# Optimization experiments

Hardware: AMD Instinct MI355X
Metric: run time of the kernel (lower is better)

Reference implementation:

```python
import jax, jax.numpy as jnp
import numpy as np

N_NODES = 100000
N_EDGES = 1600000
IN_DIM, HID_DIM, OUT_DIM = 128, 64, 64


def setup_inputs() -> dict:
    key = jax.random.key(0)
    ks = jax.random.split(key, 7)
    x = jax.random.normal(ks[0], (N_NODES, IN_DIM), dtype=jnp.float32)
    edge_index = jax.random.randint(ks[1], (2, N_EDGES), 0, N_NODES, dtype=jnp.int64)
    user_idx = jax.random.randint(ks[2], (N_NODES,), 0, N_NODES, dtype=jnp.int64)
    W1 = jax.random.normal(ks[3], (IN_DIM, HID_DIM), dtype=jnp.float32) * (1.0 / np.sqrt(IN_DIM))
    b1 = jax.random.normal(ks[4], (HID_DIM,), dtype=jnp.float32) * 0.02
    W2 = jax.random.normal(ks[5], (HID_DIM, OUT_DIM), dtype=jnp.float32) * (1.0 / np.sqrt(HID_DIM))
    b2 = jax.random.normal(ks[6], (OUT_DIM,), dtype=jnp.float32) * 0.02
    return {"x": x, "edge_index": edge_index, "user_idx": user_idx,
            "W1": W1, "b1": b1, "W2": W2, "b2": b2}


def _gcn_conv(x, edge_index, W, b):
    # PyG GCNConv: linear transform, add self-loops, sym-normalized aggregation.
    N = x.shape[0]
    h = x @ W  # [N, F_out]
    loop = jnp.arange(N, dtype=edge_index.dtype)
    src = jnp.concatenate([edge_index[0], loop])  # [E+N]
    dst = jnp.concatenate([edge_index[1], loop])
    deg = jax.ops.segment_sum(jnp.ones(src.shape[0], dtype=h.dtype), dst, num_segments=N)
    dis = jnp.where(deg > 0, jax.lax.rsqrt(jnp.maximum(deg, 1.0)), 0.0)  # deg^{-1/2}
    norm = dis[src] * dis[dst]  # [E+N]
    msg = h[src] * norm[:, None]  # gather + scale
    out = jax.ops.segment_sum(msg, dst, num_segments=N)  # scatter-add at targets
    return out + b


def _scatter_mean(x, idx, dim_size):
    s = jax.ops.segment_sum(x, idx, num_segments=dim_size)
    cnt = jax.ops.segment_sum(jnp.ones(x.shape[0], dtype=x.dtype), idx, num_segments=dim_size)
    return jnp.where(cnt[:, None] > 0, s / jnp.maximum(cnt[:, None], 1.0), 0.0)


def reference(x, edge_index, user_idx, W1, b1, W2, b2):
    h = _gcn_conv(x, edge_index, W1, b1)
    h = jax.nn.relu(h)
    # dropout is identity in eval mode
    h = _gcn_conv(h, edge_index, W2, b2)
    return _scatter_mean(h, user_idx, h.shape[0])
```

## Files before the change

### kernel.cpp

```cpp
#include <hip/hip_runtime.h>
#include <hip/hip_bf16.h>


#define FEAT 64
#define INDIM 128

#define SCAN_BS 256
#define SCAN_ELEMS 8
#define SCAN_CHUNK (SCAN_BS * SCAN_ELEMS)

#define BIN_SHIFT 9
#define BIN_R 512
#define BIN_TILE 2048
#define BH_TILE 2048

typedef __attribute__((ext_vector_type(8))) short short8;
typedef __attribute__((ext_vector_type(4))) float f32x4;

__device__ __forceinline__ unsigned short f2bf(float f) {
    unsigned u = __float_as_uint(f);
    unsigned r = u + 0x7FFFu + ((u >> 16) & 1u);
    return (unsigned short)(r >> 16);
}
__device__ __forceinline__ float bf2f(unsigned short v) {
    return __uint_as_float(((unsigned)v) << 16);
}


__global__ __launch_bounds__(256) void k_bhist(const int* __restrict__ dst,
                                               int* __restrict__ gbc,
                                               const int* __restrict__ uidx,
                                               float* __restrict__ cntf,
                                               int E, int N, int KB) {
    __shared__ int h[256];
    const int tid = threadIdx.x;
    h[tid] = 0;
    __syncthreads();
    const int base = blockIdx.x * BH_TILE;
    #pragma unroll
    for (int t = 0; t < BH_TILE / 256; ++t) {
        int e = base + t * 256 + tid;
        if (e < E) {
            int d = dst[e];
            if ((unsigned)d < (unsigned)N) atomicAdd(&h[d >> BIN_SHIFT], 1);
        }
    }
    int i = blockIdx.x * 256 + tid;
    if (i < N) {
        int u = uidx[i];
        if ((unsigned)u < (unsigned)N) atomicAdd(&cntf[u], 1.0f);
    }
    __syncthreads();
    if (tid < KB && h[tid]) atomicAdd(&gbc[tid], h[tid]);
}

__global__ __launch_bounds__(256) void k_bscan(const int* __restrict__ gbc,
                                               int* __restrict__ bb,
                                               int* __restrict__ bcur,
                                               int* __restrict__ rpN, int KB) {
    __shared__ int lds[256];
    const int tid = threadIdx.x;
    int v = (tid < KB) ? gbc[tid] : 0;
    lds[tid] = v;
    __syncthreads();
    for (int d = 1; d < 256; d <<= 1) {
        int t = (tid >= d) ? lds[tid - d] : 0;
        __syncthreads();
        lds[tid] += t;
        __syncthreads();
    }
    int excl = lds[tid] - v;
    if (tid < KB) { bb[tid] = excl; bcur[tid] = excl; }
    if (tid == 255) { bb[KB] = lds[255]; *rpN = lds[255]; }
}

__global__ __launch_bounds__(256) void k_binA(const int* __restrict__ src,
                                              const int* __restrict__ dst,
                                              int* __restrict__ bcur,
                                              unsigned* __restrict__ pairs,
                                              int E, int N, int KB) {
    __shared__ unsigned lbuf[BIN_TILE];
    __shared__ unsigned short bkt[BIN_TILE];
    __shared__ int lcnt[256];
    __shared__ int loff[256];
    __shared__ int lbase[256];
    __shared__ int tot;
    const int tid = threadIdx.x;
    const int base = blockIdx.x * BIN_TILE;

    lcnt[tid] = 0;
    __syncthreads();

    int mys[BIN_TILE / 256], myd[BIN_TILE / 256], myb[BIN_TILE / 256];
    #pragma unroll
    for (int t = 0; t < BIN_TILE / 256; ++t) {
        int e = base + t * 256 + tid;
        int s = 0, d = -1;
        if (e < E) { s = src[e]; d = dst[e]; }
        if ((unsigned)d >= (unsigned)N) d = -1;
        if ((unsigned)s >= (unsigned)N) s = 0;
        mys[t] = s; myd[t] = d;
        myb[t] = (d >= 0) ? (d >> BIN_SHIFT) : -1;
        if (myb[t] >= 0) atomicAdd(&lcnt[myb[t]], 1);
    }
    __syncthreads();

    int v = lcnt[tid];
    loff[tid] = v;
    __syncthreads();
    for (int d = 1; d < 256; d <<= 1) {
        int t2 = (tid >= d) ? loff[tid - d] : 0;
        __syncthreads();
        loff[tid] += t2;
        __syncthreads();
    }
    if (tid == 255) tot = loff[255];
    int excl = loff[tid] - v;
    __syncthreads();
    loff[tid] = excl;
    lcnt[tid] = excl;
    if (tid < KB && v > 0) lbase[tid] = atomicAdd(&bcur[tid], v);
    __syncthreads();

    #pragma unroll
    for (int t = 0; t < BIN_TILE / 256; ++t) {
        if (myb[t] >= 0) {
            int pos = atomicAdd(&lcnt[myb[t]], 1);
            lbuf[pos] = ((unsigned)mys[t] << BIN_SHIFT) | (unsigned)(myd[t] & (BIN_R - 1));
            bkt[pos] = (unsigned short)myb[t];
        }
    }
    __syncthreads();

    const int T = tot;
    for (int i = tid; i < T; i += 256) {
        int b = bkt[i];
        pairs[lbase[b] + (i - loff[b])] = lbuf[i];
    }
}

__global__ __launch_bounds__(1024) void k_binB2(const unsigned* __restrict__ pairs,
                                                const int* __restrict__ bb,
                                                int* __restrict__ rp,
                                                int* __restrict__ col,
                                                float* __restrict__ dis, int N) {
    __shared__ int cnt[BIN_R];
    __shared__ int cur[BIN_R];
    __shared__ int ssum[256];
    const int tid = threadIdx.x;
    const int b = blockIdx.x;
    const int n0 = b << BIN_SHIFT;
    const int n1 = min(n0 + BIN_R, N);
    const int nn = n1 - n0;
    const int e0 = bb[b];
    const int e1 = bb[b + 1];

    for (int i = tid; i < nn; i += 1024) cnt[i] = 0;
    __syncthreads();
    for (int i = e0 + tid; i < e1; i += 1024) {
        atomicAdd(&cnt[pairs[i] & (BIN_R - 1)], 1);
    }
    __syncthreads();

    const int i0 = 2 * tid;
    int c0 = 0, c1 = 0;
    if (tid < 256) {
        c0 = (i0     < nn) ? cnt[i0]     : 0;
        c1 = (i0 + 1 < nn) ? cnt[i0 + 1] : 0;
        ssum[tid] = c0 + c1;
    }
    __syncthreads();
    for (int d = 1; d < 256; d <<= 1) {
        int t = 0;
        if (tid < 256 && tid >= d) t = ssum[tid - d];
        __syncthreads();
        if (tid < 256) ssum[tid] += t;
        __syncthreads();
    }
    if (tid < 256) {
        int excl = ssum[tid] - (c0 + c1);
        if (i0 < nn) {
            cur[i0] = e0 + excl;
            rp[n0 + i0] = e0 + excl;
            dis[n0 + i0] = rsqrtf((float)c0 + 1.0f);
        }
        if (i0 + 1 < nn) {
            cur[i0 + 1] = e0 + excl + c0;
            rp[n0 + i0 + 1] = e0 + excl + c0;
            dis[n0 + i0 + 1] = rsqrtf((float)c1 + 1.0f);
        }
    }
    __syncthreads();

    for (int i = e0 + tid; i < e1; i += 1024) {
        unsigned p = pairs[i];
        int pos = atomicAdd(&cur[p & (BIN_R - 1)], 1);
        col[pos] = (int)(p >> BIN_SHIFT);
    }
}


__global__ __launch_bounds__(256) void k_hist(const int* __restrict__ dst,
                                              int* __restrict__ cntE, int E, int N) {
    int e = blockIdx.x * 256 + threadIdx.x;
    if (e < E) {
        int d = dst[e];
        if ((unsigned)d < (unsigned)N) atomicAdd(&cntE[d], 1);
    }
}
__global__ __launch_bounds__(256) void k_dis(const int* __restrict__ cntE,
                                             float* __restrict__ dis, int N) {
    int i = blockIdx.x * 256 + threadIdx.x;
    if (i < N) dis[i] = rsqrtf((float)cntE[i] + 1.0f);
}
__global__ __launch_bounds__(SCAN_BS) void k_scan1(const int* __restrict__ c,
                                                   int* __restrict__ rp,
                                                   int* __restrict__ ptot, int N) {
    __shared__ int lds[SCAN_BS];
    const int base = blockIdx.x * SCAN_CHUNK;
    const int tb = base + threadIdx.x * SCAN_ELEMS;
    int vals[SCAN_ELEMS];
    int s = 0;
    #pragma unroll
    for (int k = 0; k < SCAN_ELEMS; ++k) {
        int idx = tb + k;
        int v = (idx < N) ? c[idx] : 0;
        vals[k] = s;
        s += v;
    }
    lds[threadIdx.x] = s;
    __syncthreads();
    for (int d = 1; d < SCAN_BS; d <<= 1) {
        int v = (threadIdx.x >= d) ? lds[threadIdx.x - d] : 0;
        __syncthreads();
        lds[threadIdx.x] += v;
        __syncthreads();
    }
    int toff = (threadIdx.x == 0) ? 0 : lds[threadIdx.x - 1];
    #pragma unroll
    for (int k = 0; k < SCAN_ELEMS; ++k) {
        int idx = tb + k;
        if (idx < N) rp[idx] = toff + vals[k];
    }
    if (threadIdx.x == SCAN_BS - 1) ptot[blockIdx.x] = lds[SCAN_BS - 1];
}
__global__ __launch_bounds__(1024) void k_scan2(int* __restrict__ ptot,
                                                int* __restrict__ poff,
                                                int* __restrict__ rpN, int nb) {
    __shared__ int lds[1024];
    int tid = threadIdx.x;
    lds[tid] = (tid < nb) ? ptot[tid] : 0;
    __syncthreads();
    for (int d = 1; d < 1024; d <<= 1) {
        int v = (tid >= d) ? lds[tid - d] : 0;
        __syncthreads();
        lds[tid] += v;
        __syncthreads();
    }
    if (tid < nb) poff[tid] = (tid == 0) ? 0 : lds[tid - 1];
    if (tid == nb - 1) *rpN = lds[tid];
}
__global__ __launch_bounds__(SCAN_BS) void k_scan3(int* __restrict__ rp,
                                                   const int* __restrict__ poff, int N) {
    int off = poff[blockIdx.x];
    const int tb = blockIdx.x * SCAN_CHUNK + threadIdx.x * SCAN_ELEMS;
    #pragma unroll
    for (int k = 0; k < SCAN_ELEMS; ++k) {
        int idx = tb + k;
        if (idx < N) rp[idx] += off;
    }
}
__global__ __launch_bounds__(256) void k_fill(const int* __restrict__ src,
                                              const int* __restrict__ dst,
                                              const int* __restrict__ rp,
                                              int* __restrict__ tmp,
                                              int* __restrict__ col, int E, int N) {
    int e = blockIdx.x * 256 + threadIdx.x;
    if (e >= E) return;
    int s = src[e], d = dst[e];
    if ((unsigned)s >= (unsigned)N) s = 0;
    if ((unsigned)d >= (unsigned)N) return;
    int r = atomicAdd(&tmp[d], 1);
    col[rp[d] + r] = s;
}

__global__ __launch_bounds__(256) void k_ucnt(const int* __restrict__ uidx,
                                              float* __restrict__ cntf, int N) {
    int i = blockIdx.x * 256 + threadIdx.x;
    if (i < N) {
        int u = uidx[i];
        if ((unsigned)u < (unsigned)N) atomicAdd(&cntf[u], 1.0f);
    }
}


__global__ __launch_bounds__(256) void k_gemm1(const float* __restrict__ x,
                                               const float* __restrict__ W,
                                               const float* __restrict__ scale,
                                               unsigned short* __restrict__ out, int N) {
    __shared__ short wf[4 * 4 * 64 * 8];
    const int tid = threadIdx.x;
    if (blockIdx.x == 0 && tid < 8) {
        uint4 z; z.x = 0; z.y = 0; z.z = 0; z.w = 0;
        *reinterpret_cast<uint4*>(out + (long)N * FEAT + tid * 8) = z;
    }
    for (int i = tid; i < INDIM * FEAT; i += 256) {
        int k = i >> 6, n = i & 63;
        int ct = n >> 4, kc = k >> 5, r = k & 31;
        int owner = ((r >> 3) << 4) | (n & 15);
        wf[(((ct << 2) | kc) * 64 + owner) * 8 + (r & 7)] = (short)f2bf(W[i]);
    }
    __syncthreads();

    const int lane = tid & 63;
    const int m = lane & 15, q = lane >> 4;
    const int row0 = blockIdx.x * 64 + (tid >> 6) * 16;

    short8 bfr[4][4];
    #pragma unroll
    for (int ct = 0; ct < 4; ++ct)
        #pragma unroll
        for (int kc = 0; kc < 4; ++kc)
            bfr[ct][kc] = *reinterpret_cast<const short8*>(&wf[(((ct << 2) | kc) * 64 + lane) * 8]);

    int gr = row0 + m;
    int rl = gr < N ? gr : (N - 1);
    const float* xp = x + (long)rl * INDIM + q * 8;

    f32x4 acc[4] = {{0,0,0,0},{0,0,0,0},{0,0,0,0},{0,0,0,0}};
    #pragma unroll
    for (int kc = 0; kc < 4; ++kc) {
        float4 v0 = *reinterpret_cast<const float4*>(xp + kc * 32);
        float4 v1 = *reinterpret_cast<const float4*>(xp + kc * 32 + 4);
        short8 a;
        a[0]=(short)f2bf(v0.x); a[1]=(short)f2bf(v0.y); a[2]=(short)f2bf(v0.z); a[3]=(short)f2bf(v0.w);
        a[4]=(short)f2bf(v1.x); a[5]=(short)f2bf(v1.y); a[6]=(short)f2bf(v1.z); a[7]=(short)f2bf(v1.w);
        #pragma unroll
        for (int ct = 0; ct < 4; ++ct)
            acc[ct] = __builtin_amdgcn_mfma_f32_16x16x32_bf16(a, bfr[ct][kc], acc[ct], 0, 0, 0);
    }

    #pragma unroll
    for (int reg = 0; reg < 4; ++reg) {
        int row = row0 + q * 4 + reg;
        if (row < N) {
            float sc = scale[row];
            #pragma unroll
            for (int ct = 0; ct < 4; ++ct)
                out[(long)row * FEAT + ct * 16 + m] = f2bf(acc[ct][reg] * sc);
        }
    }
}

__global__ __launch_bounds__(256) void k_gemm2(const unsigned short* __restrict__ h,
                                               const float* __restrict__ W,
                                               const float* __restrict__ scale,
                                               unsigned short* __restrict__ out, int N) {
    __shared__ short wf[4 * 2 * 64 * 8];
    const int tid = threadIdx.x;
    if (blockIdx.x == 0 && tid < 8) {
        uint4 z; z.x = 0; z.y = 0; z.z = 0; z.w = 0;
        *reinterpret_cast<uint4*>(out + (long)N * FEAT + tid * 8) = z;
    }
    for (int i = tid; i < FEAT * FEAT; i += 256) {
        int k = i >> 6, n = i & 63;
        int ct = n >> 4, kc = k >> 5, r = k & 31;
        int owner = ((r >> 3) << 4) | (n & 15);
        wf[(((ct << 1) | kc) * 64 + owner) * 8 + (r & 7)] = (short)f2bf(W[i]);
    }
    __syncthreads();

    const int lane = tid & 63;
    const int m = lane & 15, q = lane >> 4;
    const int row0 = blockIdx.x * 64 + (tid >> 6) * 16;

    short8 bfr[4][2];
    #pragma unroll
    for (int ct = 0; ct < 4; ++ct)
        #pragma unroll
        for (int kc = 0; kc < 2; ++kc)
            bfr[ct][kc] = *reinterpret_cast<const short8*>(&wf[(((ct << 1) | kc) * 64 + lane) * 8]);

    int gr = row0 + m;
    int rl = gr < N ? gr : (N - 1);
    const unsigned short* hp = h + (long)rl * FEAT + q * 8;

    f32x4 acc[4] = {{0,0,0,0},{0,0,0,0},{0,0,0,0},{0,0,0,0}};
    #pragma unroll
    for (int kc = 0; kc < 2; ++kc) {
        short8 a = *reinterpret_cast<const short8*>(hp + kc * 32);
        #pragma unroll
        for (int ct = 0; ct < 4; ++ct)
            acc[ct] = __builtin_amdgcn_mfma_f32_16x16x32_bf16(a, bfr[ct][kc], acc[ct], 0, 0, 0);
    }

    #pragma unroll
    for (int reg = 0; reg < 4; ++reg) {
        int row = row0 + q * 4 + reg;
        if (row < N) {
            float sc = scale[row];
            #pragma unroll
            for (int ct = 0; ct < 4; ++ct)
                out[(long)row * FEAT + ct * 16 + m] = f2bf(acc[ct][reg] * sc);
        }
    }
}


#define ACC8(r)                                                                  \
    a0 += bf2f((unsigned short)(r).x);                                           \
    a1 += bf2f((unsigned short)((r).x >> 16));                                   \
    a2 += bf2f((unsigned short)(r).y);                                           \
    a3 += bf2f((unsigned short)((r).y >> 16));                                   \
    a4 += bf2f((unsigned short)(r).z);                                           \
    a5 += bf2f((unsigned short)((r).z >> 16));                                   \
    a6 += bf2f((unsigned short)(r).w);                                           \
    a7 += bf2f((unsigned short)((r).w >> 16));

#define AGG_BODY(SELF_INIT)                                                      \
    const int lane = threadIdx.x & 63;                                           \
    const int wv = threadIdx.x >> 6;                                             \
    const int p  = lane >> 4;                                                    \
    const int s  = (lane >> 3) & 1;                                              \
    const int ol = lane & 7;                                                     \
    const int i  = blockIdx.x * 16 + wv * 4 + p;                                 \
    const bool valid = (i < N);                                                  \
    const int jb = valid ? rp[i] : 0;                                            \
    const int je = valid ? rp[i + 1] : 0;                                        \
    float a0=0.f,a1=0.f,a2=0.f,a3=0.f,a4=0.f,a5=0.f,a6=0.f,a7=0.f;               \
    if (valid && s == 0) { SELF_INIT }                                           \
    for (int j0 = jb; j0 < je; j0 += 16) {                                       \
        int j1 = j0 + s;                                                         \
        int c1 = (j1      < je) ? col[j1]      : N;                              \
        int c2 = (j1 + 2  < je) ? col[j1 + 2]  : N;                              \
        int c3 = (j1 + 4  < je) ? col[j1 + 4]  : N;                              \
        int c4 = (j1 + 6  < je) ? col[j1 + 6]  : N;                              \
        int c5 = (j1 + 8  < je) ? col[j1 + 8]  : N;                              \
        int c6 = (j1 + 10 < je) ? col[j1 + 10] : N;                              \
        int c7 = (j1 + 12 < je) ? col[j1 + 12] : N;                              \
        int c8 = (j1 + 14 < je) ? col[j1 + 14] : N;                              \
        uint4 r1 = *reinterpret_cast<const uint4*>(A + (long)c1 * FEAT + 8 * ol);\
        uint4 r2 = *reinterpret_cast<const uint4*>(A + (long)c2 * FEAT + 8 * ol);\
        uint4 r3 = *reinterpret_cast<const uint4*>(A + (long)c3 * FEAT + 8 * ol);\
        uint4 r4 = *reinterpret_cast<const uint4*>(A + (long)c4 * FEAT + 8 * ol);\
        uint4 r5 = *reinterpret_cast<const uint4*>(A + (long)c5 * FEAT + 8 * ol);\
        uint4 r6 = *reinterpret_cast<const uint4*>(A + (long)c6 * FEAT + 8 * ol);\
        uint4 r7 = *reinterpret_cast<const uint4*>(A + (long)c7 * FEAT + 8 * ol);\
        uint4 r8 = *reinterpret_cast<const uint4*>(A + (long)c8 * FEAT + 8 * ol);\
        ACC8(r1)                                                                 \
        ACC8(r2)                                                                 \
        ACC8(r3)                                                                 \
        ACC8(r4)                                                                 \
        ACC8(r5)                                                                 \
        ACC8(r6)                                                                 \
        ACC8(r7)                                                                 \
        ACC8(r8)                                                                 \
    }                                                                            \
    a0 += __shfl_xor(a0, 8);  a1 += __shfl_xor(a1, 8);                           \
    a2 += __shfl_xor(a2, 8);  a3 += __shfl_xor(a3, 8);                           \
    a4 += __shfl_xor(a4, 8);  a5 += __shfl_xor(a5, 8);                           \
    a6 += __shfl_xor(a6, 8);  a7 += __shfl_xor(a7, 8);

__global__ __launch_bounds__(256) void k_agg1(const unsigned short* __restrict__ A,
                                              const int* __restrict__ rp,
                                              const int* __restrict__ col,
                                              const float* __restrict__ dis,
                                              const float* __restrict__ bias,
                                              unsigned short* __restrict__ H, int N) {
    AGG_BODY(
        uint4 rv = *reinterpret_cast<const uint4*>(A + (long)i * FEAT + 8 * ol);
        a0 = bf2f((unsigned short)rv.x); a1 = bf2f((unsigned short)(rv.x >> 16));
        a2 = bf2f((unsigned short)rv.y); a3 = bf2f((unsigned short)(rv.y >> 16));
        a4 = bf2f((unsigned short)rv.z); a5 = bf2f((unsigned short)(rv.z >> 16));
        a6 = bf2f((unsigned short)rv.w); a7 = bf2f((unsigned short)(rv.w >> 16));
    )
    if (s == 0 && valid) {
        float di = dis[i];
        float4 b4a = *reinterpret_cast<const float4*>(bias + 8 * ol);
        float4 b4b = *reinterpret_cast<const float4*>(bias + 8 * ol + 4);
        uint4 o;
        o.x = (unsigned)f2bf(fmaxf(fmaf(di, a0, b4a.x), 0.f))
            | ((unsigned)f2bf(fmaxf(fmaf(di, a1, b4a.y), 0.f)) << 16);
        o.y = (unsigned)f2bf(fmaxf(fmaf(di, a2, b4a.z), 0.f))
            | ((unsigned)f2bf(fmaxf(fmaf(di, a3, b4a.w), 0.f)) << 16);
        o.z = (unsigned)f2bf(fmaxf(fmaf(di, a4, b4b.x), 0.f))
            | ((unsigned)f2bf(fmaxf(fmaf(di, a5, b4b.y), 0.f)) << 16);
        o.w = (unsigned)f2bf(fmaxf(fmaf(di, a6, b4b.z), 0.f))
            | ((unsigned)f2bf(fmaxf(fmaf(di, a7, b4b.w), 0.f)) << 16);
        *reinterpret_cast<uint4*>(H + (long)i * FEAT + 8 * ol) = o;
    }
}

__global__ __launch_bounds__(256) void k_agg2s(const unsigned short* __restrict__ A,
                                               const int* __restrict__ rp,
                                               const int* __restrict__ col,
                                               const float* __restrict__ dis,
                                               const float* __restrict__ bias,
                                               const int* __restrict__ uidx,
                                               const float* __restrict__ cntf,
                                               float* __restrict__ S, int N) {
    __shared__ float sbuf[4][4][65];
    AGG_BODY(
        uint4 rv = *reinterpret_cast<const uint4*>(A + (long)i * FEAT + 8 * ol);
        a0 = bf2f((unsigned short)rv.x); a1 = bf2f((unsigned short)(rv.x >> 16));
        a2 = bf2f((unsigned short)rv.y); a3 = bf2f((unsigned short)(rv.y >> 16));
        a4 = bf2f((unsigned short)rv.z); a5 = bf2f((unsigned short)(rv.z >> 16));
        a6 = bf2f((unsigned short)rv.w); a7 = bf2f((unsigned short)(rv.w >> 16));
    )
    if (s == 0) {
        float* dl = &sbuf[wv][p][8 * ol];
        dl[0] = a0; dl[1] = a1; dl[2] = a2; dl[3] = a3;
        dl[4] = a4; dl[5] = a5; dl[6] = a6; dl[7] = a7;
    }
    __syncthreads();
    const int base4 = blockIdx.x * 16 + wv * 4;
    const float bl = bias[lane];
    #pragma unroll
    for (int pp = 0; pp < 4; ++pp) {
        int node = base4 + pp;
        if (node < N) {
            int u = uidx[node];
            if ((unsigned)u < (unsigned)N) {
                float c = cntf[u];
                float wgt = (c > 0.f) ? (1.0f / c) : 0.f;
                float di = dis[node];
                float v = sbuf[wv][pp][lane];
                atomicAdd(&S[(long)u * FEAT + lane], wgt * fmaf(di, v, bl));
            }
        }
    }
}

extern "C" void kernel_launch(void* const* d_in, const int* in_sizes, int n_in,
                              void* d_out, int out_size, void* d_ws, size_t ws_size,
                              hipStream_t stream) {
    const float* x   = (const float*)d_in[0];
    const int* edge  = (const int*)d_in[1];
    const int* uidx  = (const int*)d_in[2];
    const float* W1  = (const float*)d_in[3];
    const float* b1  = (const float*)d_in[4];
    const float* W2  = (const float*)d_in[5];
    const float* b2  = (const float*)d_in[6];
    float* out       = (float*)d_out;

    const int N = in_sizes[2];
    const int E = in_sizes[1] / 2;
    const int* src = edge;
    const int* dst = edge + E;

    const size_t fbuf = (size_t)N * FEAT * sizeof(float);
    const size_t abuf = (size_t)(N + 1) * FEAT * sizeof(unsigned short);
    const int gE   = (E + 255) / 256;
    const int gN   = (N + 255) / 256;
    const int gN16 = (N + 15) / 16;
    const int gG   = (N + 63) / 64;
    const int nbScan = (N + SCAN_CHUNK - 1) / SCAN_CHUNK;
    const int KB = (N + BIN_R - 1) >> BIN_SHIFT;

    auto align256 = [](size_t v) { return (v + 255) & ~(size_t)255; };

    char* w = (char*)d_ws;
    size_t o = 0;
    float* dis  = (float*)(w + o); o = align256(o + (size_t)N * 4);
    float* cntf = (float*)(w + o); o = align256(o + (size_t)N * 4);
    int*   rp   = (int*)  (w + o); o = align256(o + (size_t)(N + 1) * 4);
    int*   cntE = (int*)  (w + o); o = align256(o + (size_t)N * 4);
    int*   ptot = (int*)  (w + o); o = align256(o + (size_t)1024 * 4);
    int*   poff = (int*)  (w + o); o = align256(o + (size_t)1024 * 4);
    int*   col  = (int*)  (w + o); o = align256(o + (size_t)E * 4);
    size_t apsz = (size_t)E * 4 > abuf ? (size_t)E * 4 : abuf;
    char*  Ap   = w + o;           o = align256(o + apsz);
    const size_t need = o;
    int* gbc  = cntE;
    int* bb   = ptot;
    int* bcur = poff;
    unsigned* pairs = (unsigned*)Ap;
    unsigned short* A = (unsigned short*)Ap;
    unsigned short* Hb = (unsigned short*)out;

    if (ws_size >= need && KB <= 256 && N <= (1 << (32 - BIN_SHIFT - 1))) {
        hipMemsetAsync(gbc, 0, (size_t)KB * 4, stream);
        hipMemsetAsync(cntf, 0, (size_t)N * 4, stream);
        k_bhist<<<(E + BH_TILE - 1) / BH_TILE, 256, 0, stream>>>(dst, gbc, uidx, cntf, E, N, KB);
        k_bscan<<<1, 256, 0, stream>>>(gbc, bb, bcur, rp + N, KB);
        k_binA <<<(E + BIN_TILE - 1) / BIN_TILE, 256, 0, stream>>>(src, dst, bcur, pairs, E, N, KB);
        k_binB2<<<KB, 1024, 0, stream>>>(pairs, bb, rp, col, dis, N);

        k_gemm1<<<gG, 256, 0, stream>>>(x, W1, dis, A, N);
        k_agg1 <<<gN16, 256, 0, stream>>>(A, rp, col, dis, b1, Hb, N);

        k_gemm2<<<gG, 256, 0, stream>>>(Hb, W2, dis, A, N);
        hipMemsetAsync(out, 0, fbuf, stream);
        k_agg2s<<<gN16, 256, 0, stream>>>(A, rp, col, dis, b2, uidx, cntf, out, N);
    } else {
        hipMemsetAsync(cntE, 0, (size_t)N * 4, stream);
        k_hist <<<gE, 256, 0, stream>>>(dst, cntE, E, N);
        k_dis  <<<gN, 256, 0, stream>>>(cntE, dis, N);
        k_scan1<<<nbScan, SCAN_BS, 0, stream>>>(cntE, rp, ptot, N);
        k_scan2<<<1, 1024, 0, stream>>>(ptot, poff, rp + N, nbScan);
        k_scan3<<<nbScan, SCAN_BS, 0, stream>>>(rp, poff, N);
        hipMemsetAsync(cntE, 0, (size_t)N * 4, stream);
        k_fill <<<gE, 256, 0, stream>>>(src, dst, rp, cntE, col, E, N);
        hipMemsetAsync(cntf, 0, (size_t)N * 4, stream);
        k_ucnt <<<gN, 256, 0, stream>>>(uidx, cntf, N);
        k_gemm1<<<gG, 256, 0, stream>>>(x, W1, dis, A, N);
        k_agg1 <<<gN16, 256, 0, stream>>>(A, rp, col, dis, b1, Hb, N);
        k_gemm2<<<gG, 256, 0, stream>>>(Hb, W2, dis, A, N);
        hipMemsetAsync(out, 0, fbuf, stream);
        k_agg2s<<<gN16, 256, 0, stream>>>(A, rp, col, dis, b2, uidx, cntf, out, N);
    }
}
```

Measured before the change: 276.1 us.

## Fuse layer-2 GEMM into layer-1 aggregation and fold output zeroing into histogram

Adds k_agg1f, which aggregates layer 1, applies bias and ReLU into shared memory, then multiplies by W2 with MFMA bf16 instructions and writes the scaled layer-2 input into a new workspace buffer. This removes the separate k_gemm2 launch and the global round trip of the hidden activations. The output zeroing memset moves into the k_bhist grid-stride loop, and the two small memsets become one contiguous memset after the workspace is reordered. It needs an extra workspace buffer and keeps the old path as a fallback when the workspace is too small. Each agg block now reloads and repacks all of W2 into shared memory.

```diff
diff --git a/kernel.cpp b/kernel.cpp
--- a/kernel.cpp
+++ b/kernel.cpp
@@ -31,6 +31,7 @@
                                                int* __restrict__ gbc,
                                                const int* __restrict__ uidx,
                                                float* __restrict__ cntf,
+                                               uint4* __restrict__ outz, long nz4,
                                                int E, int N, int KB) {
     __shared__ int h[256];
     const int tid = threadIdx.x;
@@ -49,6 +50,12 @@
     if (i < N) {
         int u = uidx[i];
         if ((unsigned)u < (unsigned)N) atomicAdd(&cntf[u], 1.0f);
+    }
+    if (outz) {
+        uint4 z; z.x = 0; z.y = 0; z.z = 0; z.w = 0;
+        const long stride = (long)gridDim.x * 256;
+        for (long idx = (long)blockIdx.x * 256 + tid; idx < nz4; idx += stride)
+            outz[idx] = z;
     }
     __syncthreads();
     if (tid < KB && h[tid]) atomicAdd(&gbc[tid], h[tid]);
@@ -491,6 +498,74 @@
     }
 }
 
+__global__ __launch_bounds__(256) void k_agg1f(const unsigned short* __restrict__ A,
+                                               const int* __restrict__ rp,
+                                               const int* __restrict__ col,
+                                               const float* __restrict__ dis,
+                                               const float* __restrict__ bias,
+                                               const float* __restrict__ W2,
+                                               unsigned short* __restrict__ A2, int N) {
+    __shared__ short wf[4 * 2 * 64 * 8];
+    __shared__ unsigned short hh[16][72];
+    __shared__ float dl[16];
+    const int tid = threadIdx.x;
+    for (int ii = tid; ii < FEAT * FEAT; ii += 256) {
+        int k = ii >> 6, n = ii & 63;
+        int ct = n >> 4, kc = k >> 5, r = k & 31;
+        int owner = ((r >> 3) << 4) | (n & 15);
+        wf[(((ct << 1) | kc) * 64 + owner) * 8 + (r & 7)] = (short)f2bf(W2[ii]);
+    }
+    const int base16 = blockIdx.x * 16;
+    if (tid < 16) {
+        int node = base16 + tid;
+        dl[tid] = (node < N) ? dis[node] : 0.f;
+    }
+    if (blockIdx.x == 0 && tid >= 32 && tid < 40) {
+        uint4 z; z.x = 0; z.y = 0; z.z = 0; z.w = 0;
+        *reinterpret_cast<uint4*>(A2 + (long)N * FEAT + (tid - 32) * 8) = z;
+    }
+
+    AGG_BODY(
+        uint4 rv = *reinterpret_cast<const uint4*>(A + (long)i * FEAT + 8 * ol);
+        a0 = bf2f((unsigned short)rv.x); a1 = bf2f((unsigned short)(rv.x >> 16));
+        a2 = bf2f((unsigned short)rv.y); a3 = bf2f((unsigned short)(rv.y >> 16));
+        a4 = bf2f((unsigned short)rv.z); a5 = bf2f((unsigned short)(rv.z >> 16));
+        a6 = bf2f((unsigned short)rv.w); a7 = bf2f((unsigned short)(rv.w >> 16));
+    )
+    if (s == 0 && valid) {
+        float di = dis[i];
+        float4 b4a = *reinterpret_cast<const float4*>(bias + 8 * ol);
+        float4 b4b = *reinterpret_cast<const float4*>(bias + 8 * ol + 4);
+        uint4 o;
+        o.x = (unsigned)f2bf(fmaxf(fmaf(di, a0, b4a.x), 0.f))
+            | ((unsigned)f2bf(fmaxf(fmaf(di, a1, b4a.y), 0.f)) << 16);
+        o.y = (unsigned)f2bf(fmaxf(fmaf(di, a2, b4a.z), 0.f))
+            | ((unsigned)f2bf(fmaxf(fmaf(di, a3, b4a.w), 0.f)) << 16);
+        o.z = (unsigned)f2bf(fmaxf(fmaf(di, a4, b4b.x), 0.f))
+            | ((unsigned)f2bf(fmaxf(fmaf(di, a5, b4b.y), 0.f)) << 16);
+        o.w = (unsigned)f2bf(fmaxf(fmaf(di, a6, b4b.z), 0.f))
+            | ((unsigned)f2bf(fmaxf(fmaf(di, a7, b4b.w), 0.f)) << 16);
+        *reinterpret_cast<uint4*>(&hh[wv * 4 + p][8 * ol]) = o;
+    }
+    __syncthreads();
+
+    const int m = lane & 15, q = lane >> 4;
+    short8 af0 = *reinterpret_cast<const short8*>(&hh[m][q * 8]);
+    short8 af1 = *reinterpret_cast<const short8*>(&hh[m][32 + q * 8]);
+    short8 bf0 = *reinterpret_cast<const short8*>(&wf[(((wv << 1) | 0) * 64 + lane) * 8]);
+    short8 bf1 = *reinterpret_cast<const short8*>(&wf[(((wv << 1) | 1) * 64 + lane) * 8]);
+    f32x4 acc = {0, 0, 0, 0};
+    acc = __builtin_amdgcn_mfma_f32_16x16x32_bf16(af0, bf0, acc, 0, 0, 0);
+    acc = __builtin_amdgcn_mfma_f32_16x16x32_bf16(af1, bf1, acc, 0, 0, 0);
+    #pragma unroll
+    for (int reg = 0; reg < 4; ++reg) {
+        int node = q * 4 + reg;
+        int row = base16 + node;
+        if (row < N)
+            A2[(long)row * FEAT + wv * 16 + m] = f2bf(acc[reg] * dl[node]);
+    }
+}
+
 __global__ __launch_bounds__(256) void k_agg2s(const unsigned short* __restrict__ A,
                                                const int* __restrict__ rp,
                                                const int* __restrict__ col,
@@ -508,9 +583,9 @@
         a6 = bf2f((unsigned short)rv.w); a7 = bf2f((unsigned short)(rv.w >> 16));
     )
     if (s == 0) {
-        float* dl = &sbuf[wv][p][8 * ol];
-        dl[0] = a0; dl[1] = a1; dl[2] = a2; dl[3] = a3;
-        dl[4] = a4; dl[5] = a5; dl[6] = a6; dl[7] = a7;
+        float* dst = &sbuf[wv][p][8 * ol];
+        dst[0] = a0; dst[1] = a1; dst[2] = a2; dst[3] = a3;
+        dst[4] = a4; dst[5] = a5; dst[6] = a6; dst[7] = a7;
     }
     __syncthreads();
     const int base4 = blockIdx.x * 16 + wv * 4;
@@ -554,6 +629,7 @@
     const int gN   = (N + 255) / 256;
     const int gN16 = (N + 15) / 16;
     const int gG   = (N + 63) / 64;
+    const int gBH  = (E + BH_TILE - 1) / BH_TILE;
     const int nbScan = (N + SCAN_CHUNK - 1) / SCAN_CHUNK;
     const int KB = (N + BIN_R - 1) >> BIN_SHIFT;
 
@@ -563,14 +639,17 @@
     size_t o = 0;
     float* dis  = (float*)(w + o); o = align256(o + (size_t)N * 4);
     float* cntf = (float*)(w + o); o = align256(o + (size_t)N * 4);
+    int*   cntE = (int*)  (w + o); o = align256(o + (size_t)N * 4);
     int*   rp   = (int*)  (w + o); o = align256(o + (size_t)(N + 1) * 4);
-    int*   cntE = (int*)  (w + o); o = align256(o + (size_t)N * 4);
     int*   ptot = (int*)  (w + o); o = align256(o + (size_t)1024 * 4);
     int*   poff = (int*)  (w + o); o = align256(o + (size_t)1024 * 4);
     int*   col  = (int*)  (w + o); o = align256(o + (size_t)E * 4);
     size_t apsz = (size_t)E * 4 > abuf ? (size_t)E * 4 : abuf;
     char*  Ap   = w + o;           o = align256(o + apsz);
-    const size_t need = o;
+    const size_t need_base = o;
+    unsigned short* A2 = (unsigned short*)(w + o); o = align256(o + abuf);
+    const size_t need_fused = o;
+
     int* gbc  = cntE;
     int* bb   = ptot;
     int* bcur = poff;
@@ -578,17 +657,32 @@
     unsigned short* A = (unsigned short*)Ap;
     unsigned short* Hb = (unsigned short*)out;
 
-    if (ws_size >= need && KB <= 256 && N <= (1 << (32 - BIN_SHIFT - 1))) {
-        hipMemsetAsync(gbc, 0, (size_t)KB * 4, stream);
-        hipMemsetAsync(cntf, 0, (size_t)N * 4, stream);
-        k_bhist<<<(E + BH_TILE - 1) / BH_TILE, 256, 0, stream>>>(dst, gbc, uidx, cntf, E, N, KB);
+    const bool binOK = (KB <= 256) && (N <= (1 << (32 - BIN_SHIFT - 1)));
+    const long NF4 = (long)N * FEAT / 4;
+
+    if (ws_size >= need_fused && binOK) {
+        size_t zspan = (size_t)((char*)gbc - (char*)cntf) + (size_t)KB * 4;
+        hipMemsetAsync(cntf, 0, zspan, stream);
+        k_bhist<<<gBH, 256, 0, stream>>>(dst, gbc, uidx, cntf,
+                                         (uint4*)out, NF4, E, N, KB);
         k_bscan<<<1, 256, 0, stream>>>(gbc, bb, bcur, rp + N, KB);
         k_binA <<<(E + BIN_TILE - 1) / BIN_TILE, 256, 0, stream>>>(src, dst, bcur, pairs, E, N, KB);
         k_binB2<<<KB, 1024, 0, stream>>>(pairs, bb, rp, col, dis, N);
 
         k_gemm1<<<gG, 256, 0, stream>>>(x, W1, dis, A, N);
+        k_agg1f<<<gN16, 256, 0, stream>>>(A, rp, col, dis, b1, W2, A2, N);
+        k_agg2s<<<gN16, 256, 0, stream>>>(A2, rp, col, dis, b2, uidx, cntf, out, N);
+    } else if (ws_size >= need_base && binOK) {
+        size_t zspan = (size_t)((char*)gbc - (char*)cntf) + (size_t)KB * 4;
+        hipMemsetAsync(cntf, 0, zspan, stream);
+        k_bhist<<<gBH, 256, 0, stream>>>(dst, gbc, uidx, cntf,
+                                         (uint4*)nullptr, 0, E, N, KB);
+        k_bscan<<<1, 256, 0, stream>>>(gbc, bb, bcur, rp + N, KB);
+        k_binA <<<(E + BIN_TILE - 1) / BIN_TILE, 256, 0, stream>>>(src, dst, bcur, pairs, E, N, KB);
+        k_binB2<<<KB, 1024, 0, stream>>>(pairs, bb, rp, col, dis, N);
+
+        k_gemm1<<<gG, 256, 0, stream>>>(x, W1, dis, A, N);
         k_agg1 <<<gN16, 256, 0, stream>>>(A, rp, col, dis, b1, Hb, N);
-
         k_gemm2<<<gG, 256, 0, stream>>>(Hb, W2, dis, A, N);
         hipMemsetAsync(out, 0, fbuf, stream);
         k_agg2s<<<gN16, 256, 0, stream>>>(A, rp, col, dis, b2, uidx, cntf, out, N);
```

New measurement: 259.2 us. -6.1%, faster.
